# Kernel tuning notes

Measured on AMD Instinct MI355X. Metric: run time of the kernel, lower is better.

Reference implementation:

```python
import jax, jax.numpy as jnp
import numpy as np

TEMPERATURE = 1.0


def setup_inputs() -> dict:
    key = jax.random.key(0)
    kx, kw = jax.random.split(key)
    x = jax.random.normal(kx, (16, 4096, 256), dtype=jnp.float32)
    weight = jax.random.normal(kw, (1024, 256), dtype=jnp.float32)  # codebook [K, D]
    return {"x": x, "weight": weight}


def reference(x, weight):
    K, D = weight.shape
    in_shape = x.shape
    h = x.reshape(-1, D)  # [N, D]
    # distance = -mean((w - h)^2, -1) = -(|h|^2 + |w|^2 - 2 h.w) / D  (avoids N*K*D delta)
    x_sq = jnp.sum(h * h, axis=-1, keepdims=True)          # [N, 1]
    w_sq = jnp.sum(weight * weight, axis=-1)               # [K]
    cross = h @ weight.T                                   # [N, K]
    distance = -(x_sq + w_sq[None, :] - 2.0 * cross) / D   # [N, K]
    q_distribution = jax.nn.softmax(distance / TEMPERATURE, axis=-1)
    # detach_distributioin_grad=True default
    q_distribution = jax.lax.stop_gradient(q_distribution)
    quantized = q_distribution @ weight                     # [N, D]
    return (quantized.reshape(in_shape),
            q_distribution.reshape(*in_shape[:-1], K))
```

## Files before the change

### kernel.cpp

```cpp
#include <hip/hip_runtime.h>
#include <hip/hip_bf16.h>

#define DD 256
#define KC 1024
#define NT 32

typedef __attribute__((ext_vector_type(4))) float f32x4;
typedef __attribute__((ext_vector_type(8))) short bf16x8;

#define BAR() do { \
    asm volatile("s_waitcnt lgkmcnt(0)" ::: "memory"); \
    __builtin_amdgcn_s_barrier(); \
    __builtin_amdgcn_sched_barrier(0); \
} while (0)

static __device__ __forceinline__ short f2bf(float f) {
    union { float f; unsigned u; } v; v.f = f;
    unsigned u = v.u;
    unsigned r = u + 0x7fffu + ((u >> 16) & 1u);
    return (short)(r >> 16);
}
static __device__ __forceinline__ float bf2f(short s) {
    union { unsigned u; float f; } v;
    v.u = ((unsigned)(unsigned short)s) << 16;
    return v.f;
}
static __device__ __forceinline__ unsigned pk2(float a, float b) {
    return (unsigned)(unsigned short)f2bf(a) |
           ((unsigned)(unsigned short)f2bf(b) << 16);
}

__global__ void prep_kernel(const float* __restrict__ w, short* __restrict__ wbf,
                            short* __restrict__ wtbf, float* __restrict__ wsq) {
    const int cod = blockIdx.x;
    const int d   = threadIdx.x;
    float v = w[cod * DD + d];
    short b = f2bf(v);
    wbf[cod * DD + d] = b;
    wtbf[d * KC + cod] = b;
    float s = v * v;
    #pragma unroll
    for (int m = 32; m >= 1; m >>= 1) s += __shfl_xor(s, m, 64);
    __shared__ float ps[4];
    const int wave = threadIdx.x >> 6, lane = threadIdx.x & 63;
    if (lane == 0) ps[wave] = s;
    __syncthreads();
    if (threadIdx.x == 0) {
        wsq[cod] = (ps[0] + ps[1] + ps[2] + ps[3]) * (1.0f / (float)DD);
    }
}

__global__ __launch_bounds__(512, 2) void fused_kernel(
    const float* __restrict__ x, const short* __restrict__ wbf,
    const short* __restrict__ wtbf, const float* __restrict__ wsq,
    float* __restrict__ qdist, float* __restrict__ quant)
{
    __shared__ short wt_[2][32 * DD];
    __shared__ short wtT_[2][128 * 64];
    __shared__ short et_[2][64 * 36];
    __shared__ float red_[2][64];
    __shared__ float invs_[64];

    const int t   = threadIdx.x;
    const int w   = t >> 6, l = t & 63;
    const int lhi = l >> 4, llo = l & 15;
    const int rg  = w >> 1, cg = w & 1;
    const long rowbase = (long)blockIdx.x * 64;

    const int sc  = t >> 4;
    const int sg0 = (t & 15) * 2;
    const int sd  = t >> 1;
    const int sg2 = (t & 1) * 2;
    const int ssr = sd >> 1;
    const int shb = (sd & 1) * 4;

    bf16x8 wpf0, wpf1;
    float wscur, wsnext;

    { const short* p = wbf + (size_t)sc * DD + sg0 * 8;
      wpf0 = *(const bf16x8*)p; wpf1 = *(const bf16x8*)(p + 8); }

    bf16x8 xa[8];
    {
        const float* xr = x + (rowbase + rg * 16 + llo) * DD + lhi * 8;
        #pragma unroll
        for (int kk = 0; kk < 8; kk++) {
            f32x4 v0 = *(const f32x4*)(xr + kk * 32);
            f32x4 v1 = *(const f32x4*)(xr + kk * 32 + 4);
            bf16x8 b;
            b[0]=f2bf(v0[0]); b[1]=f2bf(v0[1]); b[2]=f2bf(v0[2]); b[3]=f2bf(v0[3]);
            b[4]=f2bf(v1[0]); b[5]=f2bf(v1[1]); b[6]=f2bf(v1[2]); b[7]=f2bf(v1[3]);
            xa[kk] = b;
        }
    }

    *(bf16x8*)((char*)wt_[0] + sc*512 + (((sg0    ) ^ (sc&7)) << 4)) = wpf0;
    *(bf16x8*)((char*)wt_[0] + sc*512 + (((sg0 + 1) ^ (sc&7)) << 4)) = wpf1;
    { const short* p = wbf + (size_t)(32 + sc) * DD + sg0 * 8;
      wpf0 = *(const bf16x8*)p; wpf1 = *(const bf16x8*)(p + 8); }
    wscur  = wsq[cg * 16 + llo];
    wsnext = wsq[32 + cg * 16 + llo];

    const int  mycode = cg * 16 + llo;
    const int  cswz   = mycode & 7;
    char* const wtb0  = (char*)wt_[0] + mycode * 512;
    char* const wtb1  = (char*)wt_[1] + mycode * 512;

    float rs[4] = {0.f, 0.f, 0.f, 0.f};
    unsigned epk[NT][2];

    #pragma unroll
    for (int i = 0; i < NT; i++) {
        BAR();
        if (i < NT - 1) {
            char* wb = (char*)wt_[(i + 1) & 1] + sc * 512;
            *(bf16x8*)(wb + (((sg0    ) ^ (sc&7)) << 4)) = wpf0;
            *(bf16x8*)(wb + (((sg0 + 1) ^ (sc&7)) << 4)) = wpf1;
        }
        if (i < NT - 2) {
            const short* p = wbf + (size_t)((i + 2) * 32 + sc) * DD + sg0 * 8;
            wpf0 = *(const bf16x8*)p; wpf1 = *(const bf16x8*)(p + 8);
        }
        char* wb2 = (i & 1) ? wtb1 : wtb0;
        f32x4 sacc = {0.f, 0.f, 0.f, 0.f};
        #pragma unroll
        for (int kk = 0; kk < 8; kk++) {
            bf16x8 bb = *(const bf16x8*)(wb2 + (((kk * 4 + lhi) ^ cswz) << 4));
            sacc = __builtin_amdgcn_mfma_f32_16x16x32_bf16(xa[kk], bb, sacc, 0, 0, 0);
        }
        float e0 = __expf(sacc[0] * (1.0f / 128.0f) - wscur);
        float e1 = __expf(sacc[1] * (1.0f / 128.0f) - wscur);
        float e2 = __expf(sacc[2] * (1.0f / 128.0f) - wscur);
        float e3 = __expf(sacc[3] * (1.0f / 128.0f) - wscur);
        rs[0] += e0; rs[1] += e1; rs[2] += e2; rs[3] += e3;
        epk[i][0] = pk2(e0, e1);
        epk[i][1] = pk2(e2, e3);
        wscur = wsnext;
        if (i < NT - 2) wsnext = wsq[(i + 2) * 32 + cg * 16 + llo];
    }

    bf16x8 tpf0, tpf1;
    { const short* p = wtbf + (size_t)sd * KC + sg2 * 8;
      tpf0 = *(const bf16x8*)p; tpf1 = *(const bf16x8*)(p + 8); }

    #pragma unroll
    for (int m = 1; m <= 8; m <<= 1)
        #pragma unroll
        for (int r = 0; r < 4; r++) rs[r] += __shfl_xor(rs[r], m, 64);
    if (llo == 0) {
        #pragma unroll
        for (int r = 0; r < 4; r++) red_[cg][rg * 16 + lhi * 4 + r] = rs[r];
    }
    __syncthreads();
    if (t < 64) invs_[t] = 1.0f / (red_[0][t] + red_[1][t]);
    __syncthreads();

    float inv4[4];
    #pragma unroll
    for (int r = 0; r < 4; r++) inv4[r] = invs_[rg * 16 + lhi * 4 + r];

    f32x4 uacc[4][2];
    #pragma unroll
    for (int a = 0; a < 4; a++)
        #pragma unroll
        for (int b = 0; b < 2; b++) uacc[a][b] = (f32x4){0.f, 0.f, 0.f, 0.f};

    float* qbase = qdist + rowbase * KC;
    const int myrow0 = rg * 16 + lhi * 4;
    const int qrow = t >> 3, c4 = (t & 7) * 4;

    #pragma unroll
    for (int i = 0; i < NT; i++) {
        const int b = i & 1;
        float q0 = bf2f((short)(epk[i][0] & 0xffff)) * inv4[0];
        float q1 = bf2f((short)(epk[i][0] >> 16))    * inv4[1];
        float q2 = bf2f((short)(epk[i][1] & 0xffff)) * inv4[2];
        float q3 = bf2f((short)(epk[i][1] >> 16))    * inv4[3];
        et_[b][(myrow0 + 0) * 36 + mycode] = f2bf(q0);
        et_[b][(myrow0 + 1) * 36 + mycode] = f2bf(q1);
        et_[b][(myrow0 + 2) * 36 + mycode] = f2bf(q2);
        et_[b][(myrow0 + 3) * 36 + mycode] = f2bf(q3);
        {
            char* tb = (char*)wtT_[b] + ssr * 128;
            *(bf16x8*)(tb + (((shb + sg2    ) ^ (ssr & 7)) << 4)) = tpf0;
            *(bf16x8*)(tb + (((shb + sg2 + 1) ^ (ssr & 7)) << 4)) = tpf1;
        }
        if (i < NT - 1) {
            const short* p = wtbf + (size_t)sd * KC + (i + 1) * 32 + sg2 * 8;
            tpf0 = *(const bf16x8*)p; tpf1 = *(const bf16x8*)(p + 8);
        }
        BAR();
        {
            const char* ep = (const char*)et_[b] + qrow * 72 + c4 * 2;
            unsigned u0 = *(const unsigned*)ep;
            unsigned u1 = *(const unsigned*)(ep + 4);
            f32x4 o;
            o[0] = bf2f((short)(u0 & 0xffff)); o[1] = bf2f((short)(u0 >> 16));
            o[2] = bf2f((short)(u1 & 0xffff)); o[3] = bf2f((short)(u1 >> 16));
            *(f32x4*)(qbase + (size_t)qrow * KC + (size_t)i * 32 + c4) = o;
        }
        bf16x8 bb0, bb1;
        {
            const int d0 = w * 32 + llo;
            bb0 = *(const bf16x8*)((char*)wtT_[b] + (d0 >> 1) * 128 +
                    (((((d0 & 1) << 2) + lhi) ^ ((d0 >> 1) & 7)) << 4));
            const int d1 = w * 32 + 16 + llo;
            bb1 = *(const bf16x8*)((char*)wtT_[b] + (d1 >> 1) * 128 +
                    (((((d1 & 1) << 2) + lhi) ^ ((d1 >> 1) & 7)) << 4));
        }
        #pragma unroll
        for (int rowg = 0; rowg < 4; rowg++) {
            bf16x8 aa = *(const bf16x8*)((char*)et_[b] + (rowg * 16 + llo) * 72 + lhi * 16);
            uacc[rowg][0] = __builtin_amdgcn_mfma_f32_16x16x32_bf16(bb0, aa, uacc[rowg][0], 0, 0, 0);
            uacc[rowg][1] = __builtin_amdgcn_mfma_f32_16x16x32_bf16(bb1, aa, uacc[rowg][1], 0, 0, 0);
        }
    }

    #pragma unroll
    for (int rowg = 0; rowg < 4; rowg++)
        #pragma unroll
        for (int dg = 0; dg < 2; dg++)
            *(f32x4*)(quant + (rowbase + rowg * 16 + llo) * DD + w * 32 + dg * 16 + lhi * 4)
                = uacc[rowg][dg];
}

extern "C" void kernel_launch(void* const* d_in, const int* in_sizes, int n_in,
                              void* d_out, int out_size, void* d_ws, size_t ws_size,
                              hipStream_t stream) {
    const float* x = (const float*)d_in[0];
    const float* w = (const float*)d_in[1];
    float* out = (float*)d_out;

    const int nrows = in_sizes[0] / DD;
    float* quant = out;
    float* qdist = out + (size_t)nrows * DD;

    short* wbf  = (short*)d_ws;
    short* wtbf = wbf + (size_t)KC * DD;
    float* wsq  = (float*)(wtbf + (size_t)DD * KC);

    prep_kernel<<<KC, DD, 0, stream>>>(w, wbf, wtbf, wsq);
    fused_kernel<<<nrows / 64, 512, 0, stream>>>(x, wbf, wtbf, wsq, qdist, quant);
}
```

Before: 174.7 us.

## Load codebook MFMA operands directly from global into registers, drop LDS staging

Both GEMM phases now load each wave's bf16 codebook MFMA B-operands straight from global memory (L2-resident) into registers, double-buffered across tiles, instead of staging shared tiles through swizzled LDS. This removes the per-tile barrier and LDS round-trip in the score loop, and it frees most of the LDS. In exchange, each wave redundantly fetches the weights its neighbours also use, which raises L2 traffic and register pressure under the 512-thread, 2-blocks launch bound. Global latency may also be exposed when only one tile is prefetched ahead.

```diff
diff --git a/kernel.cpp b/kernel.cpp
--- a/kernel.cpp
+++ b/kernel.cpp
@@ -7,6 +7,8 @@
 
 typedef __attribute__((ext_vector_type(4))) float f32x4;
 typedef __attribute__((ext_vector_type(8))) short bf16x8;
+
+#define MFMA16 __builtin_amdgcn_mfma_f32_16x16x32_bf16
 
 #define BAR() do { \
     asm volatile("s_waitcnt lgkmcnt(0)" ::: "memory"); \
@@ -50,13 +52,80 @@
     }
 }
 
+#define LOADW(W0,W1,W2,W3,W4,W5,W6,W7, TILE) do { \
+    const short* _p = wbf + ((size_t)((TILE) * 32) + cg * 16 + llo) * DD + lhi * 8; \
+    W0 = *(const bf16x8*)(_p      ); W1 = *(const bf16x8*)(_p +  32); \
+    W2 = *(const bf16x8*)(_p +  64); W3 = *(const bf16x8*)(_p +  96); \
+    W4 = *(const bf16x8*)(_p + 128); W5 = *(const bf16x8*)(_p + 160); \
+    W6 = *(const bf16x8*)(_p + 192); W7 = *(const bf16x8*)(_p + 224); \
+} while (0)
+
+#define SCOREMM(W0,W1,W2,W3,W4,W5,W6,W7, SACC) do { \
+    SACC = (f32x4){0.f,0.f,0.f,0.f}; \
+    SACC = MFMA16(xa[0], W0, SACC, 0,0,0); \
+    SACC = MFMA16(xa[1], W1, SACC, 0,0,0); \
+    SACC = MFMA16(xa[2], W2, SACC, 0,0,0); \
+    SACC = MFMA16(xa[3], W3, SACC, 0,0,0); \
+    SACC = MFMA16(xa[4], W4, SACC, 0,0,0); \
+    SACC = MFMA16(xa[5], W5, SACC, 0,0,0); \
+    SACC = MFMA16(xa[6], W6, SACC, 0,0,0); \
+    SACC = MFMA16(xa[7], W7, SACC, 0,0,0); \
+} while (0)
+
+#define EXPST(SACC, I) do { \
+    float _e0 = __expf(SACC[0] * (1.0f/128.0f) - wscur); \
+    float _e1 = __expf(SACC[1] * (1.0f/128.0f) - wscur); \
+    float _e2 = __expf(SACC[2] * (1.0f/128.0f) - wscur); \
+    float _e3 = __expf(SACC[3] * (1.0f/128.0f) - wscur); \
+    rs[0] += _e0; rs[1] += _e1; rs[2] += _e2; rs[3] += _e3; \
+    epk[I][0] = pk2(_e0, _e1); epk[I][1] = pk2(_e2, _e3); \
+    wscur = wsnext; \
+    if ((I) + 2 < NT) wsnext = wsq[((I) + 2) * 32 + cg * 16 + llo]; \
+} while (0)
+
+#define LOADPB(B0,B1, TILE) do { \
+    const short* _p = wtbf + (size_t)(w * 32 + llo) * KC + (TILE) * 32 + lhi * 8; \
+    B0 = *(const bf16x8*)_p; \
+    B1 = *(const bf16x8*)(_p + (size_t)16 * KC); \
+} while (0)
+
+#define PVSTEP(B0,B1, I) do { \
+    const int _b = (I) & 1; \
+    float _q0 = bf2f((short)(epk[I][0] & 0xffff)) * inv4[0]; \
+    float _q1 = bf2f((short)(epk[I][0] >> 16))    * inv4[1]; \
+    float _q2 = bf2f((short)(epk[I][1] & 0xffff)) * inv4[2]; \
+    float _q3 = bf2f((short)(epk[I][1] >> 16))    * inv4[3]; \
+    et_[_b][(myrow0 + 0) * 36 + mycode] = f2bf(_q0); \
+    et_[_b][(myrow0 + 1) * 36 + mycode] = f2bf(_q1); \
+    et_[_b][(myrow0 + 2) * 36 + mycode] = f2bf(_q2); \
+    et_[_b][(myrow0 + 3) * 36 + mycode] = f2bf(_q3); \
+    BAR(); \
+    {  \
+      const char* _ep = (const char*)et_[_b] + qrow * 72 + c4 * 2; \
+      unsigned _u0 = *(const unsigned*)_ep, _u1 = *(const unsigned*)(_ep + 4); \
+      f32x4 _o; \
+      _o[0] = bf2f((short)(_u0 & 0xffff)); _o[1] = bf2f((short)(_u0 >> 16)); \
+      _o[2] = bf2f((short)(_u1 & 0xffff)); _o[3] = bf2f((short)(_u1 >> 16)); \
+      *(f32x4*)(qbase + (size_t)qrow * KC + (size_t)(I) * 32 + c4) = _o; } \
+    { bf16x8 _a0 = *(const bf16x8*)((char*)et_[_b] + (      llo) * 72 + lhi * 16); \
+      bf16x8 _a1 = *(const bf16x8*)((char*)et_[_b] + (16 + llo) * 72 + lhi * 16); \
+      bf16x8 _a2 = *(const bf16x8*)((char*)et_[_b] + (32 + llo) * 72 + lhi * 16); \
+      bf16x8 _a3 = *(const bf16x8*)((char*)et_[_b] + (48 + llo) * 72 + lhi * 16); \
+      uacc[0][0] = MFMA16(B0, _a0, uacc[0][0], 0,0,0); \
+      uacc[0][1] = MFMA16(B1, _a0, uacc[0][1], 0,0,0); \
+      uacc[1][0] = MFMA16(B0, _a1, uacc[1][0], 0,0,0); \
+      uacc[1][1] = MFMA16(B1, _a1, uacc[1][1], 0,0,0); \
+      uacc[2][0] = MFMA16(B0, _a2, uacc[2][0], 0,0,0); \
+      uacc[2][1] = MFMA16(B1, _a2, uacc[2][1], 0,0,0); \
+      uacc[3][0] = MFMA16(B0, _a3, uacc[3][0], 0,0,0); \
+      uacc[3][1] = MFMA16(B1, _a3, uacc[3][1], 0,0,0); } \
+} while (0)
+
 __global__ __launch_bounds__(512, 2) void fused_kernel(
     const float* __restrict__ x, const short* __restrict__ wbf,
     const short* __restrict__ wtbf, const float* __restrict__ wsq,
     float* __restrict__ qdist, float* __restrict__ quant)
 {
-    __shared__ short wt_[2][32 * DD];
-    __shared__ short wtT_[2][128 * 64];
     __shared__ short et_[2][64 * 36];
     __shared__ float red_[2][64];
     __shared__ float invs_[64];
@@ -67,18 +136,14 @@
     const int rg  = w >> 1, cg = w & 1;
     const long rowbase = (long)blockIdx.x * 64;
 
-    const int sc  = t >> 4;
-    const int sg0 = (t & 15) * 2;
-    const int sd  = t >> 1;
-    const int sg2 = (t & 1) * 2;
-    const int ssr = sd >> 1;
-    const int shb = (sd & 1) * 4;
-
-    bf16x8 wpf0, wpf1;
-    float wscur, wsnext;
-
-    { const short* p = wbf + (size_t)sc * DD + sg0 * 8;
-      wpf0 = *(const bf16x8*)p; wpf1 = *(const bf16x8*)(p + 8); }
+    const int mycode = cg * 16 + llo;
+    const int myrow0 = rg * 16 + lhi * 4;
+    const int qrow = t >> 3, c4 = (t & 7) * 4;
+
+    bf16x8 wA0,wA1,wA2,wA3,wA4,wA5,wA6,wA7;
+    bf16x8 wB0,wB1,wB2,wB3,wB4,wB5,wB6,wB7;
+    LOADW(wA0,wA1,wA2,wA3,wA4,wA5,wA6,wA7, 0);
+    LOADW(wB0,wB1,wB2,wB3,wB4,wB5,wB6,wB7, 1);
 
     bf16x8 xa[8];
     {
@@ -94,54 +159,26 @@
         }
     }
 
-    *(bf16x8*)((char*)wt_[0] + sc*512 + (((sg0    ) ^ (sc&7)) << 4)) = wpf0;
-    *(bf16x8*)((char*)wt_[0] + sc*512 + (((sg0 + 1) ^ (sc&7)) << 4)) = wpf1;
-    { const short* p = wbf + (size_t)(32 + sc) * DD + sg0 * 8;
-      wpf0 = *(const bf16x8*)p; wpf1 = *(const bf16x8*)(p + 8); }
-    wscur  = wsq[cg * 16 + llo];
-    wsnext = wsq[32 + cg * 16 + llo];
-
-    const int  mycode = cg * 16 + llo;
-    const int  cswz   = mycode & 7;
-    char* const wtb0  = (char*)wt_[0] + mycode * 512;
-    char* const wtb1  = (char*)wt_[1] + mycode * 512;
+    float wscur  = wsq[cg * 16 + llo];
+    float wsnext = wsq[32 + cg * 16 + llo];
 
     float rs[4] = {0.f, 0.f, 0.f, 0.f};
     unsigned epk[NT][2];
 
-    #pragma unroll
-    for (int i = 0; i < NT; i++) {
-        BAR();
-        if (i < NT - 1) {
-            char* wb = (char*)wt_[(i + 1) & 1] + sc * 512;
-            *(bf16x8*)(wb + (((sg0    ) ^ (sc&7)) << 4)) = wpf0;
-            *(bf16x8*)(wb + (((sg0 + 1) ^ (sc&7)) << 4)) = wpf1;
-        }
-        if (i < NT - 2) {
-            const short* p = wbf + (size_t)((i + 2) * 32 + sc) * DD + sg0 * 8;
-            wpf0 = *(const bf16x8*)p; wpf1 = *(const bf16x8*)(p + 8);
-        }
-        char* wb2 = (i & 1) ? wtb1 : wtb0;
-        f32x4 sacc = {0.f, 0.f, 0.f, 0.f};
-        #pragma unroll
-        for (int kk = 0; kk < 8; kk++) {
-            bf16x8 bb = *(const bf16x8*)(wb2 + (((kk * 4 + lhi) ^ cswz) << 4));
-            sacc = __builtin_amdgcn_mfma_f32_16x16x32_bf16(xa[kk], bb, sacc, 0, 0, 0);
-        }
-        float e0 = __expf(sacc[0] * (1.0f / 128.0f) - wscur);
-        float e1 = __expf(sacc[1] * (1.0f / 128.0f) - wscur);
-        float e2 = __expf(sacc[2] * (1.0f / 128.0f) - wscur);
-        float e3 = __expf(sacc[3] * (1.0f / 128.0f) - wscur);
-        rs[0] += e0; rs[1] += e1; rs[2] += e2; rs[3] += e3;
-        epk[i][0] = pk2(e0, e1);
-        epk[i][1] = pk2(e2, e3);
-        wscur = wsnext;
-        if (i < NT - 2) wsnext = wsq[(i + 2) * 32 + cg * 16 + llo];
-    }
-
-    bf16x8 tpf0, tpf1;
-    { const short* p = wtbf + (size_t)sd * KC + sg2 * 8;
-      tpf0 = *(const bf16x8*)p; tpf1 = *(const bf16x8*)(p + 8); }
+    f32x4 sA, sB;
+    #pragma unroll
+    for (int i = 0; i < NT; i += 2) {
+        SCOREMM(wA0,wA1,wA2,wA3,wA4,wA5,wA6,wA7, sA);
+        if (i + 2 < NT) LOADW(wA0,wA1,wA2,wA3,wA4,wA5,wA6,wA7, i + 2);
+        EXPST(sA, i);
+        SCOREMM(wB0,wB1,wB2,wB3,wB4,wB5,wB6,wB7, sB);
+        if (i + 3 < NT) LOADW(wB0,wB1,wB2,wB3,wB4,wB5,wB6,wB7, i + 3);
+        EXPST(sB, i + 1);
+    }
+
+    bf16x8 bbA0, bbA1, bbB0, bbB1;
+    LOADPB(bbA0, bbA1, 0);
+    LOADPB(bbB0, bbB1, 1);
 
     #pragma unroll
     for (int m = 1; m <= 8; m <<= 1)
@@ -166,54 +203,13 @@
         for (int b = 0; b < 2; b++) uacc[a][b] = (f32x4){0.f, 0.f, 0.f, 0.f};
 
     float* qbase = qdist + rowbase * KC;
-    const int myrow0 = rg * 16 + lhi * 4;
-    const int qrow = t >> 3, c4 = (t & 7) * 4;
-
-    #pragma unroll
-    for (int i = 0; i < NT; i++) {
-        const int b = i & 1;
-        float q0 = bf2f((short)(epk[i][0] & 0xffff)) * inv4[0];
-        float q1 = bf2f((short)(epk[i][0] >> 16))    * inv4[1];
-        float q2 = bf2f((short)(epk[i][1] & 0xffff)) * inv4[2];
-        float q3 = bf2f((short)(epk[i][1] >> 16))    * inv4[3];
-        et_[b][(myrow0 + 0) * 36 + mycode] = f2bf(q0);
-        et_[b][(myrow0 + 1) * 36 + mycode] = f2bf(q1);
-        et_[b][(myrow0 + 2) * 36 + mycode] = f2bf(q2);
-        et_[b][(myrow0 + 3) * 36 + mycode] = f2bf(q3);
-        {
-            char* tb = (char*)wtT_[b] + ssr * 128;
-            *(bf16x8*)(tb + (((shb + sg2    ) ^ (ssr & 7)) << 4)) = tpf0;
-            *(bf16x8*)(tb + (((shb + sg2 + 1) ^ (ssr & 7)) << 4)) = tpf1;
-        }
-        if (i < NT - 1) {
-            const short* p = wtbf + (size_t)sd * KC + (i + 1) * 32 + sg2 * 8;
-            tpf0 = *(const bf16x8*)p; tpf1 = *(const bf16x8*)(p + 8);
-        }
-        BAR();
-        {
-            const char* ep = (const char*)et_[b] + qrow * 72 + c4 * 2;
-            unsigned u0 = *(const unsigned*)ep;
-            unsigned u1 = *(const unsigned*)(ep + 4);
-            f32x4 o;
-            o[0] = bf2f((short)(u0 & 0xffff)); o[1] = bf2f((short)(u0 >> 16));
-            o[2] = bf2f((short)(u1 & 0xffff)); o[3] = bf2f((short)(u1 >> 16));
-            *(f32x4*)(qbase + (size_t)qrow * KC + (size_t)i * 32 + c4) = o;
-        }
-        bf16x8 bb0, bb1;
-        {
-            const int d0 = w * 32 + llo;
-            bb0 = *(const bf16x8*)((char*)wtT_[b] + (d0 >> 1) * 128 +
-                    (((((d0 & 1) << 2) + lhi) ^ ((d0 >> 1) & 7)) << 4));
-            const int d1 = w * 32 + 16 + llo;
-            bb1 = *(const bf16x8*)((char*)wtT_[b] + (d1 >> 1) * 128 +
-                    (((((d1 & 1) << 2) + lhi) ^ ((d1 >> 1) & 7)) << 4));
-        }
-        #pragma unroll
-        for (int rowg = 0; rowg < 4; rowg++) {
-            bf16x8 aa = *(const bf16x8*)((char*)et_[b] + (rowg * 16 + llo) * 72 + lhi * 16);
-            uacc[rowg][0] = __builtin_amdgcn_mfma_f32_16x16x32_bf16(bb0, aa, uacc[rowg][0], 0, 0, 0);
-            uacc[rowg][1] = __builtin_amdgcn_mfma_f32_16x16x32_bf16(bb1, aa, uacc[rowg][1], 0, 0, 0);
-        }
+
+    #pragma unroll
+    for (int i = 0; i < NT; i += 2) {
+        PVSTEP(bbA0, bbA1, i);
+        if (i + 2 < NT) LOADPB(bbA0, bbA1, i + 2);
+        PVSTEP(bbB0, bbB1, i + 1);
+        if (i + 3 < NT) LOADPB(bbB0, bbB1, i + 3);
     }
 
     #pragma unroll
```

After: 388.8 us. 2.23x slower.

## Retile first GEMM so each wave covers 32 rows by 16 codes

Applied to the files above, without the earlier changes.

The 8 waves are regrouped into 2 row groups by 4 code groups. Each wave now holds two 16-row x fragments and reuses every codebook LDS read for two MFMAs, and each stage processes 64 codes, which halves the number of barriered iterations in the distance phase. The softmax row-sum reduction now sums four column groups, and the second phase alternates which half of the waves writes the normalized probabilities into the LDS staging tile. The trade-off is more registers per thread (doubled x fragments, a 16x2x2 packed-exp array, a 4-vector weight prefetch) and a larger LDS weight buffer, which could cost occupancy at the 512x2 launch bounds.

```diff
diff --git a/kernel.cpp b/kernel.cpp
--- a/kernel.cpp
+++ b/kernel.cpp
@@ -3,10 +3,13 @@
 
 #define DD 256
 #define KC 1024
-#define NT 32
+#define NT1 16
+#define NT2 32
 
 typedef __attribute__((ext_vector_type(4))) float f32x4;
 typedef __attribute__((ext_vector_type(8))) short bf16x8;
+
+#define MFMA16 __builtin_amdgcn_mfma_f32_16x16x32_bf16
 
 #define BAR() do { \
     asm volatile("s_waitcnt lgkmcnt(0)" ::: "memory"); \
@@ -55,34 +58,37 @@
     const short* __restrict__ wtbf, const float* __restrict__ wsq,
     float* __restrict__ qdist, float* __restrict__ quant)
 {
-    __shared__ short wt_[2][32 * DD];
+    __shared__ short wt_[2][64 * DD];
     __shared__ short wtT_[2][128 * 64];
     __shared__ short et_[2][64 * 36];
-    __shared__ float red_[2][64];
+    __shared__ float red_[4][64];
     __shared__ float invs_[64];
 
     const int t   = threadIdx.x;
     const int w   = t >> 6, l = t & 63;
     const int lhi = l >> 4, llo = l & 15;
-    const int rg  = w >> 1, cg = w & 1;
+    const int rg  = w >> 2, cg = w & 3;
     const long rowbase = (long)blockIdx.x * 64;
 
-    const int sc  = t >> 4;
-    const int sg0 = (t & 15) * 2;
+    const int sc1 = t >> 3;
+    const int gq  = (t & 7) * 4;
     const int sd  = t >> 1;
     const int sg2 = (t & 1) * 2;
     const int ssr = sd >> 1;
     const int shb = (sd & 1) * 4;
 
-    bf16x8 wpf0, wpf1;
-    float wscur, wsnext;
-
-    { const short* p = wbf + (size_t)sc * DD + sg0 * 8;
-      wpf0 = *(const bf16x8*)p; wpf1 = *(const bf16x8*)(p + 8); }
-
-    bf16x8 xa[8];
+    bf16x8 wpf[4];
+
     {
-        const float* xr = x + (rowbase + rg * 16 + llo) * DD + lhi * 8;
+        const short* p = wbf + (size_t)sc1 * DD + gq * 8;
+        #pragma unroll
+        for (int j = 0; j < 4; j++) wpf[j] = *(const bf16x8*)(p + j * 8);
+    }
+
+    bf16x8 xa[2][8];
+    #pragma unroll
+    for (int g = 0; g < 2; g++) {
+        const float* xr = x + (rowbase + rg * 32 + g * 16 + llo) * DD + lhi * 8;
         #pragma unroll
         for (int kk = 0; kk < 8; kk++) {
             f32x4 v0 = *(const f32x4*)(xr + kk * 32);
@@ -90,53 +96,67 @@
             bf16x8 b;
             b[0]=f2bf(v0[0]); b[1]=f2bf(v0[1]); b[2]=f2bf(v0[2]); b[3]=f2bf(v0[3]);
             b[4]=f2bf(v1[0]); b[5]=f2bf(v1[1]); b[6]=f2bf(v1[2]); b[7]=f2bf(v1[3]);
-            xa[kk] = b;
-        }
-    }
-
-    *(bf16x8*)((char*)wt_[0] + sc*512 + (((sg0    ) ^ (sc&7)) << 4)) = wpf0;
-    *(bf16x8*)((char*)wt_[0] + sc*512 + (((sg0 + 1) ^ (sc&7)) << 4)) = wpf1;
-    { const short* p = wbf + (size_t)(32 + sc) * DD + sg0 * 8;
-      wpf0 = *(const bf16x8*)p; wpf1 = *(const bf16x8*)(p + 8); }
-    wscur  = wsq[cg * 16 + llo];
-    wsnext = wsq[32 + cg * 16 + llo];
-
-    const int  mycode = cg * 16 + llo;
-    const int  cswz   = mycode & 7;
-    char* const wtb0  = (char*)wt_[0] + mycode * 512;
-    char* const wtb1  = (char*)wt_[1] + mycode * 512;
-
-    float rs[4] = {0.f, 0.f, 0.f, 0.f};
-    unsigned epk[NT][2];
-
-    #pragma unroll
-    for (int i = 0; i < NT; i++) {
+            xa[g][kk] = b;
+        }
+    }
+
+    #pragma unroll
+    for (int j = 0; j < 4; j++)
+        *(bf16x8*)((char*)wt_[0] + sc1 * 512 + (((gq + j) ^ (sc1 & 7)) << 4)) = wpf[j];
+    {
+        const short* p = wbf + (size_t)(64 + sc1) * DD + gq * 8;
+        #pragma unroll
+        for (int j = 0; j < 4; j++) wpf[j] = *(const bf16x8*)(p + j * 8);
+    }
+
+    const int mycode = cg * 16 + llo;
+    const int cswz   = mycode & 7;
+    float wscur  = wsq[mycode];
+    float wsnext = wsq[64 + mycode];
+
+    float rs[2][4] = {{0.f,0.f,0.f,0.f},{0.f,0.f,0.f,0.f}};
+    unsigned epk[NT1][2][2];
+
+    #pragma unroll
+    for (int i = 0; i < NT1; i++) {
         BAR();
-        if (i < NT - 1) {
-            char* wb = (char*)wt_[(i + 1) & 1] + sc * 512;
-            *(bf16x8*)(wb + (((sg0    ) ^ (sc&7)) << 4)) = wpf0;
-            *(bf16x8*)(wb + (((sg0 + 1) ^ (sc&7)) << 4)) = wpf1;
-        }
-        if (i < NT - 2) {
-            const short* p = wbf + (size_t)((i + 2) * 32 + sc) * DD + sg0 * 8;
-            wpf0 = *(const bf16x8*)p; wpf1 = *(const bf16x8*)(p + 8);
-        }
-        char* wb2 = (i & 1) ? wtb1 : wtb0;
-        f32x4 sacc = {0.f, 0.f, 0.f, 0.f};
+        if (i < NT1 - 1) {
+            char* wb = (char*)wt_[(i + 1) & 1] + sc1 * 512;
+            #pragma unroll
+            for (int j = 0; j < 4; j++)
+                *(bf16x8*)(wb + (((gq + j) ^ (sc1 & 7)) << 4)) = wpf[j];
+        }
+        if (i < NT1 - 2) {
+            const short* p = wbf + (size_t)((i + 2) * 64 + sc1) * DD + gq * 8;
+            #pragma unroll
+            for (int j = 0; j < 4; j++) wpf[j] = *(const bf16x8*)(p + j * 8);
+        }
+        char* wb2 = (char*)wt_[i & 1] + mycode * 512;
+        f32x4 s0 = {0.f,0.f,0.f,0.f}, s1 = {0.f,0.f,0.f,0.f};
         #pragma unroll
         for (int kk = 0; kk < 8; kk++) {
             bf16x8 bb = *(const bf16x8*)(wb2 + (((kk * 4 + lhi) ^ cswz) << 4));
-            sacc = __builtin_amdgcn_mfma_f32_16x16x32_bf16(xa[kk], bb, sacc, 0, 0, 0);
-        }
-        float e0 = __expf(sacc[0] * (1.0f / 128.0f) - wscur);
-        float e1 = __expf(sacc[1] * (1.0f / 128.0f) - wscur);
-        float e2 = __expf(sacc[2] * (1.0f / 128.0f) - wscur);
-        float e3 = __expf(sacc[3] * (1.0f / 128.0f) - wscur);
-        rs[0] += e0; rs[1] += e1; rs[2] += e2; rs[3] += e3;
-        epk[i][0] = pk2(e0, e1);
-        epk[i][1] = pk2(e2, e3);
+            s0 = MFMA16(xa[0][kk], bb, s0, 0, 0, 0);
+            s1 = MFMA16(xa[1][kk], bb, s1, 0, 0, 0);
+        }
+        {
+            float e0 = __expf(s0[0] * (1.0f/128.0f) - wscur);
+            float e1 = __expf(s0[1] * (1.0f/128.0f) - wscur);
+            float e2 = __expf(s0[2] * (1.0f/128.0f) - wscur);
+            float e3 = __expf(s0[3] * (1.0f/128.0f) - wscur);
+            rs[0][0] += e0; rs[0][1] += e1; rs[0][2] += e2; rs[0][3] += e3;
+            epk[i][0][0] = pk2(e0, e1); epk[i][0][1] = pk2(e2, e3);
+        }
+        {
+            float e0 = __expf(s1[0] * (1.0f/128.0f) - wscur);
+            float e1 = __expf(s1[1] * (1.0f/128.0f) - wscur);
+            float e2 = __expf(s1[2] * (1.0f/128.0f) - wscur);
+            float e3 = __expf(s1[3] * (1.0f/128.0f) - wscur);
+            rs[1][0] += e0; rs[1][1] += e1; rs[1][2] += e2; rs[1][3] += e3;
+            epk[i][1][0] = pk2(e0, e1); epk[i][1][1] = pk2(e2, e3);
+        }
         wscur = wsnext;
-        if (i < NT - 2) wsnext = wsq[(i + 2) * 32 + cg * 16 + llo];
+        if (i < NT1 - 2) wsnext = wsq[(i + 2) * 64 + mycode];
     }
 
     bf16x8 tpf0, tpf1;
@@ -146,18 +166,27 @@
     #pragma unroll
     for (int m = 1; m <= 8; m <<= 1)
         #pragma unroll
-        for (int r = 0; r < 4; r++) rs[r] += __shfl_xor(rs[r], m, 64);
+        for (int g = 0; g < 2; g++)
+            #pragma unroll
+            for (int r = 0; r < 4; r++)
+                rs[g][r] += __shfl_xor(rs[g][r], m, 64);
     if (llo == 0) {
         #pragma unroll
-        for (int r = 0; r < 4; r++) red_[cg][rg * 16 + lhi * 4 + r] = rs[r];
+        for (int g = 0; g < 2; g++)
+            #pragma unroll
+            for (int r = 0; r < 4; r++)
+                red_[cg][rg * 32 + g * 16 + lhi * 4 + r] = rs[g][r];
     }
     __syncthreads();
-    if (t < 64) invs_[t] = 1.0f / (red_[0][t] + red_[1][t]);
+    if (t < 64) invs_[t] = 1.0f / (red_[0][t] + red_[1][t] + red_[2][t] + red_[3][t]);
     __syncthreads();
 
-    float inv4[4];
-    #pragma unroll
-    for (int r = 0; r < 4; r++) inv4[r] = invs_[rg * 16 + lhi * 4 + r];
+    float inv8[2][4];
+    #pragma unroll
+    for (int g = 0; g < 2; g++)
+        #pragma unroll
+        for (int r = 0; r < 4; r++)
+            inv8[g][r] = invs_[rg * 32 + g * 16 + lhi * 4 + r];
 
     f32x4 uacc[4][2];
     #pragma unroll
@@ -166,27 +195,32 @@
         for (int b = 0; b < 2; b++) uacc[a][b] = (f32x4){0.f, 0.f, 0.f, 0.f};
 
     float* qbase = qdist + rowbase * KC;
-    const int myrow0 = rg * 16 + lhi * 4;
     const int qrow = t >> 3, c4 = (t & 7) * 4;
-
-    #pragma unroll
-    for (int i = 0; i < NT; i++) {
-        const int b = i & 1;
-        float q0 = bf2f((short)(epk[i][0] & 0xffff)) * inv4[0];
-        float q1 = bf2f((short)(epk[i][0] >> 16))    * inv4[1];
-        float q2 = bf2f((short)(epk[i][1] & 0xffff)) * inv4[2];
-        float q3 = bf2f((short)(epk[i][1] >> 16))    * inv4[3];
-        et_[b][(myrow0 + 0) * 36 + mycode] = f2bf(q0);
-        et_[b][(myrow0 + 1) * 36 + mycode] = f2bf(q1);
-        et_[b][(myrow0 + 2) * 36 + mycode] = f2bf(q2);
-        et_[b][(myrow0 + 3) * 36 + mycode] = f2bf(q3);
+    const int ci   = (cg & 1) * 16 + llo;
+    const int chalf = cg >> 1;
+
+    #pragma unroll
+    for (int k = 0; k < NT2; k++) {
+        const int b = k & 1;
+        if (chalf == (k & 1)) {
+            const int t16 = k >> 1;
+            #pragma unroll
+            for (int g = 0; g < 2; g++) {
+                const unsigned p0 = epk[t16][g][0], p1 = epk[t16][g][1];
+                const int row0 = rg * 32 + g * 16 + lhi * 4;
+                et_[b][(row0 + 0) * 36 + ci] = f2bf(bf2f((short)(p0 & 0xffff)) * inv8[g][0]);
+                et_[b][(row0 + 1) * 36 + ci] = f2bf(bf2f((short)(p0 >> 16))    * inv8[g][1]);
+                et_[b][(row0 + 2) * 36 + ci] = f2bf(bf2f((short)(p1 & 0xffff)) * inv8[g][2]);
+                et_[b][(row0 + 3) * 36 + ci] = f2bf(bf2f((short)(p1 >> 16))    * inv8[g][3]);
+            }
+        }
         {
             char* tb = (char*)wtT_[b] + ssr * 128;
             *(bf16x8*)(tb + (((shb + sg2    ) ^ (ssr & 7)) << 4)) = tpf0;
             *(bf16x8*)(tb + (((shb + sg2 + 1) ^ (ssr & 7)) << 4)) = tpf1;
         }
-        if (i < NT - 1) {
-            const short* p = wtbf + (size_t)sd * KC + (i + 1) * 32 + sg2 * 8;
+        if (k < NT2 - 1) {
+            const short* p = wtbf + (size_t)sd * KC + (k + 1) * 32 + sg2 * 8;
             tpf0 = *(const bf16x8*)p; tpf1 = *(const bf16x8*)(p + 8);
         }
         BAR();
@@ -197,7 +231,7 @@
             f32x4 o;
             o[0] = bf2f((short)(u0 & 0xffff)); o[1] = bf2f((short)(u0 >> 16));
             o[2] = bf2f((short)(u1 & 0xffff)); o[3] = bf2f((short)(u1 >> 16));
-            *(f32x4*)(qbase + (size_t)qrow * KC + (size_t)i * 32 + c4) = o;
+            *(f32x4*)(qbase + (size_t)qrow * KC + (size_t)k * 32 + c4) = o;
         }
         bf16x8 bb0, bb1;
         {
@@ -211,8 +245,8 @@
         #pragma unroll
         for (int rowg = 0; rowg < 4; rowg++) {
             bf16x8 aa = *(const bf16x8*)((char*)et_[b] + (rowg * 16 + llo) * 72 + lhi * 16);
-            uacc[rowg][0] = __builtin_amdgcn_mfma_f32_16x16x32_bf16(bb0, aa, uacc[rowg][0], 0, 0, 0);
-            uacc[rowg][1] = __builtin_amdgcn_mfma_f32_16x16x32_bf16(bb1, aa, uacc[rowg][1], 0, 0, 0);
+            uacc[rowg][0] = MFMA16(bb0, aa, uacc[rowg][0], 0, 0, 0);
+            uacc[rowg][1] = MFMA16(bb1, aa, uacc[rowg][1], 0, 0, 0);
         }
     }
 
```

After: 187.8 us. 1.08x slower.

## Halve block row tile to 32 rows with 256 threads per block

Applied to the files above, without the earlier changes.

Shrinks each block from 64 rows and 8 waves to 32 rows and 4 waves, doubling the grid. Each thread now stages four 16-byte codebook chunks instead of two, and in the second GEMM each wave covers 64 output columns over 2 row groups. The goal is more blocks in flight and better load balance across CUs. The cost is that every codebook tile is fetched from global/L2 twice as often per row, and the wider per-thread load and accumulator sets raise register pressure.

```diff
diff --git a/kernel.cpp b/kernel.cpp
--- a/kernel.cpp
+++ b/kernel.cpp
@@ -7,6 +7,8 @@
 
 typedef __attribute__((ext_vector_type(4))) float f32x4;
 typedef __attribute__((ext_vector_type(8))) short bf16x8;
+
+#define MFMA16 __builtin_amdgcn_mfma_f32_16x16x32_bf16
 
 #define BAR() do { \
     asm volatile("s_waitcnt lgkmcnt(0)" ::: "memory"); \
@@ -50,35 +52,36 @@
     }
 }
 
-__global__ __launch_bounds__(512, 2) void fused_kernel(
+__global__ __launch_bounds__(256, 2) void fused_kernel(
     const float* __restrict__ x, const short* __restrict__ wbf,
     const short* __restrict__ wtbf, const float* __restrict__ wsq,
     float* __restrict__ qdist, float* __restrict__ quant)
 {
     __shared__ short wt_[2][32 * DD];
     __shared__ short wtT_[2][128 * 64];
-    __shared__ short et_[2][64 * 36];
-    __shared__ float red_[2][64];
-    __shared__ float invs_[64];
+    __shared__ short et_[2][32 * 36];
+    __shared__ float red_[2][32];
+    __shared__ float invs_[32];
 
     const int t   = threadIdx.x;
     const int w   = t >> 6, l = t & 63;
     const int lhi = l >> 4, llo = l & 15;
     const int rg  = w >> 1, cg = w & 1;
-    const long rowbase = (long)blockIdx.x * 64;
-
-    const int sc  = t >> 4;
-    const int sg0 = (t & 15) * 2;
-    const int sd  = t >> 1;
-    const int sg2 = (t & 1) * 2;
+    const long rowbase = (long)blockIdx.x * 32;
+
+    const int sc = t >> 3;
+    const int gq = (t & 7) * 4;
+    const int sd  = t;
     const int ssr = sd >> 1;
     const int shb = (sd & 1) * 4;
 
-    bf16x8 wpf0, wpf1;
-    float wscur, wsnext;
-
-    { const short* p = wbf + (size_t)sc * DD + sg0 * 8;
-      wpf0 = *(const bf16x8*)p; wpf1 = *(const bf16x8*)(p + 8); }
+    bf16x8 wpf[4];
+
+    {
+        const short* p = wbf + (size_t)sc * DD + gq * 8;
+        #pragma unroll
+        for (int j = 0; j < 4; j++) wpf[j] = *(const bf16x8*)(p + j * 8);
+    }
 
     bf16x8 xa[8];
     {
@@ -94,17 +97,19 @@
         }
     }
 
-    *(bf16x8*)((char*)wt_[0] + sc*512 + (((sg0    ) ^ (sc&7)) << 4)) = wpf0;
-    *(bf16x8*)((char*)wt_[0] + sc*512 + (((sg0 + 1) ^ (sc&7)) << 4)) = wpf1;
-    { const short* p = wbf + (size_t)(32 + sc) * DD + sg0 * 8;
-      wpf0 = *(const bf16x8*)p; wpf1 = *(const bf16x8*)(p + 8); }
-    wscur  = wsq[cg * 16 + llo];
-    wsnext = wsq[32 + cg * 16 + llo];
-
-    const int  mycode = cg * 16 + llo;
-    const int  cswz   = mycode & 7;
-    char* const wtb0  = (char*)wt_[0] + mycode * 512;
-    char* const wtb1  = (char*)wt_[1] + mycode * 512;
+    #pragma unroll
+    for (int j = 0; j < 4; j++)
+        *(bf16x8*)((char*)wt_[0] + sc * 512 + (((gq + j) ^ (sc & 7)) << 4)) = wpf[j];
+    {
+        const short* p = wbf + (size_t)(32 + sc) * DD + gq * 8;
+        #pragma unroll
+        for (int j = 0; j < 4; j++) wpf[j] = *(const bf16x8*)(p + j * 8);
+    }
+
+    const int mycode = cg * 16 + llo;
+    const int cswz   = mycode & 7;
+    float wscur  = wsq[mycode];
+    float wsnext = wsq[32 + mycode];
 
     float rs[4] = {0.f, 0.f, 0.f, 0.f};
     unsigned epk[NT][2];
@@ -114,19 +119,21 @@
         BAR();
         if (i < NT - 1) {
             char* wb = (char*)wt_[(i + 1) & 1] + sc * 512;
-            *(bf16x8*)(wb + (((sg0    ) ^ (sc&7)) << 4)) = wpf0;
-            *(bf16x8*)(wb + (((sg0 + 1) ^ (sc&7)) << 4)) = wpf1;
+            #pragma unroll
+            for (int j = 0; j < 4; j++)
+                *(bf16x8*)(wb + (((gq + j) ^ (sc & 7)) << 4)) = wpf[j];
         }
         if (i < NT - 2) {
-            const short* p = wbf + (size_t)((i + 2) * 32 + sc) * DD + sg0 * 8;
-            wpf0 = *(const bf16x8*)p; wpf1 = *(const bf16x8*)(p + 8);
-        }
-        char* wb2 = (i & 1) ? wtb1 : wtb0;
+            const short* p = wbf + (size_t)((i + 2) * 32 + sc) * DD + gq * 8;
+            #pragma unroll
+            for (int j = 0; j < 4; j++) wpf[j] = *(const bf16x8*)(p + j * 8);
+        }
+        char* wb2 = (char*)wt_[i & 1] + mycode * 512;
         f32x4 sacc = {0.f, 0.f, 0.f, 0.f};
         #pragma unroll
         for (int kk = 0; kk < 8; kk++) {
             bf16x8 bb = *(const bf16x8*)(wb2 + (((kk * 4 + lhi) ^ cswz) << 4));
-            sacc = __builtin_amdgcn_mfma_f32_16x16x32_bf16(xa[kk], bb, sacc, 0, 0, 0);
+            sacc = MFMA16(xa[kk], bb, sacc, 0, 0, 0);
         }
         float e0 = __expf(sacc[0] * (1.0f / 128.0f) - wscur);
         float e1 = __expf(sacc[1] * (1.0f / 128.0f) - wscur);
@@ -136,12 +143,15 @@
         epk[i][0] = pk2(e0, e1);
         epk[i][1] = pk2(e2, e3);
         wscur = wsnext;
-        if (i < NT - 2) wsnext = wsq[(i + 2) * 32 + cg * 16 + llo];
-    }
-
-    bf16x8 tpf0, tpf1;
-    { const short* p = wtbf + (size_t)sd * KC + sg2 * 8;
-      tpf0 = *(const bf16x8*)p; tpf1 = *(const bf16x8*)(p + 8); }
+        if (i < NT - 2) wsnext = wsq[(i + 2) * 32 + mycode];
+    }
+
+    bf16x8 tpf[4];
+    {
+        const short* p = wtbf + (size_t)sd * KC;
+        #pragma unroll
+        for (int j = 0; j < 4; j++) tpf[j] = *(const bf16x8*)(p + j * 8);
+    }
 
     #pragma unroll
     for (int m = 1; m <= 8; m <<= 1)
@@ -152,42 +162,46 @@
         for (int r = 0; r < 4; r++) red_[cg][rg * 16 + lhi * 4 + r] = rs[r];
     }
     __syncthreads();
-    if (t < 64) invs_[t] = 1.0f / (red_[0][t] + red_[1][t]);
+    if (t < 32) invs_[t] = 1.0f / (red_[0][t] + red_[1][t]);
     __syncthreads();
 
     float inv4[4];
     #pragma unroll
     for (int r = 0; r < 4; r++) inv4[r] = invs_[rg * 16 + lhi * 4 + r];
 
-    f32x4 uacc[4][2];
-    #pragma unroll
-    for (int a = 0; a < 4; a++)
-        #pragma unroll
-        for (int b = 0; b < 2; b++) uacc[a][b] = (f32x4){0.f, 0.f, 0.f, 0.f};
+    f32x4 uacc[2][4];
+    #pragma unroll
+    for (int a = 0; a < 2; a++)
+        #pragma unroll
+        for (int b = 0; b < 4; b++) uacc[a][b] = (f32x4){0.f, 0.f, 0.f, 0.f};
 
     float* qbase = qdist + rowbase * KC;
     const int myrow0 = rg * 16 + lhi * 4;
     const int qrow = t >> 3, c4 = (t & 7) * 4;
 
     #pragma unroll
-    for (int i = 0; i < NT; i++) {
-        const int b = i & 1;
-        float q0 = bf2f((short)(epk[i][0] & 0xffff)) * inv4[0];
-        float q1 = bf2f((short)(epk[i][0] >> 16))    * inv4[1];
-        float q2 = bf2f((short)(epk[i][1] & 0xffff)) * inv4[2];
-        float q3 = bf2f((short)(epk[i][1] >> 16))    * inv4[3];
-        et_[b][(myrow0 + 0) * 36 + mycode] = f2bf(q0);
-        et_[b][(myrow0 + 1) * 36 + mycode] = f2bf(q1);
-        et_[b][(myrow0 + 2) * 36 + mycode] = f2bf(q2);
-        et_[b][(myrow0 + 3) * 36 + mycode] = f2bf(q3);
+    for (int k = 0; k < NT; k++) {
+        const int b = k & 1;
+        {
+            float q0 = bf2f((short)(epk[k][0] & 0xffff)) * inv4[0];
+            float q1 = bf2f((short)(epk[k][0] >> 16))    * inv4[1];
+            float q2 = bf2f((short)(epk[k][1] & 0xffff)) * inv4[2];
+            float q3 = bf2f((short)(epk[k][1] >> 16))    * inv4[3];
+            et_[b][(myrow0 + 0) * 36 + mycode] = f2bf(q0);
+            et_[b][(myrow0 + 1) * 36 + mycode] = f2bf(q1);
+            et_[b][(myrow0 + 2) * 36 + mycode] = f2bf(q2);
+            et_[b][(myrow0 + 3) * 36 + mycode] = f2bf(q3);
+        }
         {
             char* tb = (char*)wtT_[b] + ssr * 128;
-            *(bf16x8*)(tb + (((shb + sg2    ) ^ (ssr & 7)) << 4)) = tpf0;
-            *(bf16x8*)(tb + (((shb + sg2 + 1) ^ (ssr & 7)) << 4)) = tpf1;
-        }
-        if (i < NT - 1) {
-            const short* p = wtbf + (size_t)sd * KC + (i + 1) * 32 + sg2 * 8;
-            tpf0 = *(const bf16x8*)p; tpf1 = *(const bf16x8*)(p + 8);
+            #pragma unroll
+            for (int j = 0; j < 4; j++)
+                *(bf16x8*)(tb + (((shb + j) ^ (ssr & 7)) << 4)) = tpf[j];
+        }
+        if (k < NT - 1) {
+            const short* p = wtbf + (size_t)sd * KC + (k + 1) * 32;
+            #pragma unroll
+            for (int j = 0; j < 4; j++) tpf[j] = *(const bf16x8*)(p + j * 8);
         }
         BAR();
         {
@@ -197,30 +211,29 @@
             f32x4 o;
             o[0] = bf2f((short)(u0 & 0xffff)); o[1] = bf2f((short)(u0 >> 16));
             o[2] = bf2f((short)(u1 & 0xffff)); o[3] = bf2f((short)(u1 >> 16));
-            *(f32x4*)(qbase + (size_t)qrow * KC + (size_t)i * 32 + c4) = o;
-        }
-        bf16x8 bb0, bb1;
-        {
-            const int d0 = w * 32 + llo;
-            bb0 = *(const bf16x8*)((char*)wtT_[b] + (d0 >> 1) * 128 +
-                    (((((d0 & 1) << 2) + lhi) ^ ((d0 >> 1) & 7)) << 4));
-            const int d1 = w * 32 + 16 + llo;
-            bb1 = *(const bf16x8*)((char*)wtT_[b] + (d1 >> 1) * 128 +
-                    (((((d1 & 1) << 2) + lhi) ^ ((d1 >> 1) & 7)) << 4));
-        }
-        #pragma unroll
-        for (int rowg = 0; rowg < 4; rowg++) {
+            *(f32x4*)(qbase + (size_t)qrow * KC + (size_t)k * 32 + c4) = o;
+        }
+        bf16x8 bb[4];
+        #pragma unroll
+        for (int dg = 0; dg < 4; dg++) {
+            const int d0 = w * 64 + dg * 16 + llo;
+            bb[dg] = *(const bf16x8*)((char*)wtT_[b] + (d0 >> 1) * 128 +
+                       (((((d0 & 1) << 2) + lhi) ^ ((d0 >> 1) & 7)) << 4));
+        }
+        #pragma unroll
+        for (int rowg = 0; rowg < 2; rowg++) {
             bf16x8 aa = *(const bf16x8*)((char*)et_[b] + (rowg * 16 + llo) * 72 + lhi * 16);
-            uacc[rowg][0] = __builtin_amdgcn_mfma_f32_16x16x32_bf16(bb0, aa, uacc[rowg][0], 0, 0, 0);
-            uacc[rowg][1] = __builtin_amdgcn_mfma_f32_16x16x32_bf16(bb1, aa, uacc[rowg][1], 0, 0, 0);
-        }
-    }
-
-    #pragma unroll
-    for (int rowg = 0; rowg < 4; rowg++)
-        #pragma unroll
-        for (int dg = 0; dg < 2; dg++)
-            *(f32x4*)(quant + (rowbase + rowg * 16 + llo) * DD + w * 32 + dg * 16 + lhi * 4)
+            #pragma unroll
+            for (int dg = 0; dg < 4; dg++)
+                uacc[rowg][dg] = MFMA16(bb[dg], aa, uacc[rowg][dg], 0, 0, 0);
+        }
+    }
+
+    #pragma unroll
+    for (int rowg = 0; rowg < 2; rowg++)
+        #pragma unroll
+        for (int dg = 0; dg < 4; dg++)
+            *(f32x4*)(quant + (rowbase + rowg * 16 + llo) * DD + w * 64 + dg * 16 + lhi * 4)
                 = uacc[rowg][dg];
 }
 
@@ -240,5 +253,5 @@
     float* wsq  = (float*)(wtbf + (size_t)DD * KC);
 
     prep_kernel<<<KC, DD, 0, stream>>>(w, wbf, wtbf, wsq);
-    fused_kernel<<<nrows / 64, 512, 0, stream>>>(x, wbf, wtbf, wsq, qdist, quant);
-}
+    fused_kernel<<<nrows / 32, 256, 0, stream>>>(x, wbf, wtbf, wsq, qdist, quant);
+}
```

New measurement: 248.9 us. 1.42x slower.
